# Kernel tuning notes

Measured on AMD Instinct MI355X. Metric: run time of the kernel, lower is better.

Reference implementation:

```python
import jax, jax.numpy as jnp
import numpy as np

B = 8
RESOLUTIONS = [65, 129, 257, 513, 1025]
NUM_POINTS = [0, 4096, 16384, 65536, 262144]
CLIP_MIN = -1e9
FINAL = 1025          # last resolution (both axes)
B_MIN, B_MAX = -1.0, 1.0
BALANCE = 0.5


def setup_inputs() -> dict:
    key = jax.random.key(0)
    k1, k2, k3, k4 = jax.random.split(key, 4)
    return {
        "w1": jax.random.normal(k1, (2, 256), jnp.float32),
        "b1": jax.random.normal(k2, (256,), jnp.float32),
        "w2": jax.random.normal(k3, (256, 1), jnp.float32),
        "b2": jax.random.normal(k4, (1,), jnp.float32),
    }


def _interp_bilinear_ac(x, H, W):
    """F.interpolate(..., mode='bilinear', align_corners=True). x: [B, C, h, w]."""
    b, c, h, w = x.shape
    ys = jnp.linspace(0.0, h - 1.0, H)
    xs = jnp.linspace(0.0, w - 1.0, W)
    y0 = jnp.floor(ys).astype(jnp.int32)
    y1 = jnp.minimum(y0 + 1, h - 1)
    wy = ys - y0
    x0 = jnp.floor(xs).astype(jnp.int32)
    x1 = jnp.minimum(x0 + 1, w - 1)
    wx = xs - x0
    # interpolate rows, then columns
    top = x[:, :, y0, :] * (1.0 - wy)[None, None, :, None] + x[:, :, y1, :] * wy[None, None, :, None]
    return top[:, :, :, x0] * (1.0 - wx) + top[:, :, :, x1] * wx


def _batch_eval(coords, w1, b1, w2, b2):
    """coords: [B, N, 2] in final-resolution pixel space (align_corners=False mapping).
    Returns occupancy [B, N] (C == 1)."""
    coords2d = coords / FINAL + 0.5 / FINAL                 # normalize to [0, 1]
    p = coords2d * (B_MAX - B_MIN) + B_MIN                  # [B, N, 2] in world coords
    h = jax.nn.relu(jnp.einsum('bnd,dh->bnh', p, w1) + b1)  # [B, N, 256]
    occ = jax.nn.sigmoid(jnp.einsum('bnh,ho->bno', h, w2) + b2)
    return occ[..., 0]


def reference(w1, b1, w2, b2):
    occ = None
    for i, res in enumerate(RESOLUTIONS):
        if i == 0:
            # init_coords: grid of res x res points spanning [0, FINAL-1]
            xs = jnp.linspace(0.0, FINAL - 1.0, res)
            gy, gx = jnp.meshgrid(xs, xs, indexing='ij')          # y rows, x cols
            coords = jnp.stack([gx.ravel(), gy.ravel()], axis=-1)  # [N, 2] (x, y)
            coords = jnp.broadcast_to(coords, (B, res * res, 2))
            o = _batch_eval(coords, w1, b1, w2, b2)               # [B, N]
            occ = o.reshape(B, 1, res, res)                       # [B, C, H, W]
        else:
            occ = _interp_bilinear_ac(occ, res, res)
            npt = NUM_POINTS[i]
            if npt <= 0:
                continue
            # uncertainty = -|occ - balance_value|
            unc = -jnp.abs(occ - BALANCE)                          # [B, 1, H, W]
            flat_unc = unc.reshape(B, res * res)
            scores, idx = jax.lax.top_k(flat_unc, npt)             # [B, npt]
            px = (idx % res).astype(jnp.float32)
            py = (idx // res).astype(jnp.float32)
            stride = (FINAL - 1.0) / (res - 1.0)
            coords = jnp.stack([px, py], axis=-1) * stride         # [B, npt, 2]
            new_vals = _batch_eval(coords, w1, b1, w2, b2)         # [B, npt]
            occ_flat = occ.reshape(B, res * res)
            old_vals = jnp.take_along_axis(occ_flat, idx, axis=1)
            vals = jnp.where(scores >= CLIP_MIN, new_vals, old_vals)
            occ_flat = jax.vmap(lambda o, i2, v: o.at[i2].set(v))(occ_flat, idx, vals)
            occ = occ_flat.reshape(B, 1, res, res)
    return occ
```

## Files before the change

### kernel.cpp

```cpp
#include <hip/hip_runtime.h>
#include <stdint.h>

#define HID 256
#define NMAXPIX (1025 * 1025)
#define NREP 8
#define NSEG 2048
#define SELMAX 2112

#define HISTA_OFF 0
#define HISTB_OFF 16384
#define HISTC_OFF 32768
#define SCAL_OFF  40960
#define TIC_OFF   41024
#define STAGE_U32 43072

__device__ __forceinline__ float mlp_eval4(float wx, float wy,
                                           const float4* __restrict__ w1x,
                                           const float4* __restrict__ w1y,
                                           const float4* __restrict__ vb1,
                                           const float4* __restrict__ vw2, float b2v) {
    const float C0 = (float)(0.5 / 1025.0);
    float px = (wx / 1025.0f + C0) * 2.0f - 1.0f;
    float py = (wy / 1025.0f + C0) * 2.0f - 1.0f;
    float a0 = 0.f, a1 = 0.f, a2 = 0.f, a3 = 0.f;
#pragma unroll 8
    for (int q = 0; q < HID / 4; ++q) {
        float4 a = w1x[q], b = w1y[q], c = vb1[q], d = vw2[q];
        float h0 = px * a.x + py * b.x + c.x;
        float h1 = px * a.y + py * b.y + c.y;
        float h2 = px * a.z + py * b.z + c.z;
        float h3 = px * a.w + py * b.w + c.w;
        h0 = h0 > 0.f ? h0 : 0.f;
        h1 = h1 > 0.f ? h1 : 0.f;
        h2 = h2 > 0.f ? h2 : 0.f;
        h3 = h3 > 0.f ? h3 : 0.f;
        a0 += h0 * d.x;
        a1 += h1 * d.y;
        a2 += h2 * d.z;
        a3 += h3 * d.w;
    }
    float x = ((a0 + a1) + (a2 + a3)) + b2v;
    float r;
    if (x >= 0.f) { r = 1.0f / (1.0f + expf(-x)); }
    else { float e = expf(x); r = e / (1.0f + e); }
    return r;
}

__device__ __forceinline__ uint32_t block_exscan_256(uint32_t v, volatile uint32_t* lds4) {
    int lane = threadIdx.x & 63, w = threadIdx.x >> 6;
    uint32_t inc = v;
#pragma unroll
    for (int d = 1; d < 64; d <<= 1) {
        uint32_t o = (uint32_t)__shfl_up((int)inc, d, 64);
        if (lane >= d) inc += o;
    }
    if (lane == 63) lds4[w] = inc;
    __syncthreads();
    uint32_t woff = 0;
    for (int i = 0; i < w; ++i) woff += lds4[i];
    return woff + inc - v;
}

__device__ void scan_dev(const uint32_t* __restrict__ hist, int NB,
                         uint32_t rem_in, uint32_t prefix_in, int shift,
                         uint32_t* outp, uint32_t* outr,
                         volatile uint32_t* lds4, volatile uint32_t* ldspair) {
    int tid = threadIdx.x;
    int C = NB >> 8;
    int b0 = NB - (tid + 1) * C;
    uint32_t cnts[8];
#pragma unroll
    for (int k = 0; k < 8; ++k) cnts[k] = 0;
    for (int rep = 0; rep < NREP; ++rep) {
        const uint4* p = (const uint4*)(hist + (size_t)rep * NB + b0);
#pragma unroll
        for (int g = 0; g < 2; ++g) {
            if (g * 4 < C) {
                uint4 v = p[g];
                cnts[g * 4 + 0] += v.x;
                cnts[g * 4 + 1] += v.y;
                cnts[g * 4 + 2] += v.z;
                cnts[g * 4 + 3] += v.w;
            }
        }
    }
    uint32_t ssum = 0;
    for (int k = 0; k < C; ++k) ssum += cnts[k];
    uint32_t excl = block_exscan_256(ssum, lds4);
    uint32_t run = excl;
    for (int k = 0; k < C; ++k) {
        uint32_t c = cnts[C - 1 - k];
        if (rem_in > run && rem_in <= run + c) {
            ldspair[0] = (prefix_in << shift) | (uint32_t)(b0 + C - 1 - k);
            ldspair[1] = rem_in - run;
        }
        run += c;
    }
    __syncthreads();
    *outp = ldspair[0];
    *outr = ldspair[1];
}

__global__ __launch_bounds__(256) void k_eval0z(const float* __restrict__ w1, const float* __restrict__ b1,
                                                const float* __restrict__ w2, const float* __restrict__ b2,
                                                float* __restrict__ occ, uint32_t* __restrict__ zbuf, int zcount) {
    __shared__ alignas(16) float sw1[2 * HID];
    __shared__ alignas(16) float sb1[HID];
    __shared__ alignas(16) float sw2[HID];
    int tid = threadIdx.x;
    for (int i = tid; i < 2 * HID; i += 256) sw1[i] = w1[i];
    sb1[tid] = b1[tid];
    sw2[tid] = w2[tid];
    __syncthreads();
    int gtid = blockIdx.x * 256 + tid;
    int nthreads = gridDim.x * 256;
    for (int i = gtid; i < zcount; i += nthreads) zbuf[i] = 0;
    for (int n = gtid; n < 65 * 65; n += nthreads) {
        int i = n / 65, j = n % 65;
        occ[n] = mlp_eval4(16.0f * (float)j, 16.0f * (float)i,
                           (const float4*)sw1, (const float4*)(sw1 + HID),
                           (const float4*)sb1, (const float4*)sw2, b2[0]);
    }
}

__global__ __launch_bounds__(256) void k_upkey(const float* __restrict__ in, int rp,
                                               float* __restrict__ outg, int r, int nb, int bstride,
                                               uint32_t* __restrict__ keys,
                                               uint32_t* __restrict__ histA) {
    __shared__ uint32_t hist[2048];
    int tid = threadIdx.x;
    for (int k = tid; k < 2048; k += 256) hist[k] = 0;
    __syncthreads();
    int N = r * r;
    int lane = tid & 63;
    int gstride = gridDim.x * 256;
    for (int n0 = blockIdx.x * 256; n0 < N; n0 += gstride) {
        int n = n0 + tid;
        bool act = n < N;
        uint32_t key = 0;
        if (act) {
            int i = n / r, j = n % r;
            int i2 = i >> 1, j2 = j >> 1;
            float v;
            if ((i & 1) == 0) {
                if ((j & 1) == 0) {
                    v = in[i2 * rp + j2];
                } else {
                    float a = in[i2 * rp + j2], b = in[i2 * rp + j2 + 1];
                    v = a * 0.5f + b * 0.5f;
                }
            } else {
                if ((j & 1) == 0) {
                    float a = in[i2 * rp + j2], b = in[(i2 + 1) * rp + j2];
                    v = a * 0.5f + b * 0.5f;
                } else {
                    float a = in[i2 * rp + j2],      c = in[i2 * rp + j2 + 1];
                    float b = in[(i2 + 1) * rp + j2], d = in[(i2 + 1) * rp + j2 + 1];
                    float t1 = a * 0.5f + b * 0.5f;
                    float t2 = c * 0.5f + d * 0.5f;
                    v = t1 * 0.5f + t2 * 0.5f;
                }
            }
            for (int k = 0; k < nb; ++k) outg[(size_t)k * bstride + n] = v;
            float unc = -fabsf(v - 0.5f);
            uint32_t u = __float_as_uint(unc);
            key = (u & 0x80000000u) ? ~u : (u | 0x80000000u);
            keys[n] = key;
        }
        uint32_t bin = key >> 21;
        unsigned long long m = __ballot(act);
        if (m) {
            int leader = __ffsll(m) - 1;
            uint32_t lbin = (uint32_t)__shfl((int)bin, leader, 64);
            unsigned long long smk = __ballot(act && bin == lbin);
            if (smk == m) {
                if (lane == leader) atomicAdd(&hist[lbin], (uint32_t)__popcll(m));
            } else if (act) {
                atomicAdd(&hist[bin], 1u);
            }
        }
    }
    __syncthreads();
    uint32_t* myrep = histA + (size_t)(blockIdx.x & (NREP - 1)) * 2048;
    for (int k = tid; k < 2048; k += 256) {
        uint32_t c = hist[k];
        if (c) atomicAdd(&myrep[k], c);
    }
}

__global__ __launch_bounds__(256) void k_histmid(const uint32_t* __restrict__ keys, int N,
                                                 const uint32_t* __restrict__ prevHist,
                                                 uint32_t* __restrict__ scal,
                                                 int useNpt, uint32_t npt, int scalInIdx, int shift,
                                                 int scalOutIdx,
                                                 int fshift, int bshift, uint32_t bmask,
                                                 uint32_t* __restrict__ outHist, int NBout) {
    __shared__ uint32_t lh[2048];
    __shared__ uint32_t lds4[4];
    __shared__ uint32_t ldspair[2];
    int tid = threadIdx.x, lane = tid & 63;
    uint32_t rem_in = useNpt ? npt : scal[scalInIdx + 1];
    uint32_t pfx_in = useNpt ? 0u  : scal[scalInIdx];
    uint32_t pfx, rem;
    scan_dev(prevHist, 2048, rem_in, pfx_in, shift, &pfx, &rem, lds4, ldspair);
    if (blockIdx.x == 0 && tid == 0) { scal[scalOutIdx] = pfx; scal[scalOutIdx + 1] = rem; }
    for (int k = tid; k < 2048; k += 256) lh[k] = 0;
    __syncthreads();
    int gstride = gridDim.x * 256;
    for (int base = blockIdx.x * 256; base < N; base += gstride) {
        int n = base + tid;
        bool inb = n < N;
        uint32_t key = inb ? keys[n] : 0u;
        bool flt = inb && ((key >> fshift) == pfx);
        uint32_t bin = (key >> bshift) & bmask;
        unsigned long long m = __ballot(flt);
        if (m) {
            int leader = __ffsll(m) - 1;
            uint32_t lbin = (uint32_t)__shfl((int)bin, leader, 64);
            unsigned long long smk = __ballot(flt && bin == lbin);
            if (smk == m) {
                if (lane == leader) atomicAdd(&lh[lbin], (uint32_t)__popcll(m));
            } else if (flt) {
                atomicAdd(&lh[bin], 1u);
            }
        }
    }
    __syncthreads();
    uint32_t* myrep = outHist + (size_t)(blockIdx.x & (NREP - 1)) * NBout;
    for (int k = tid; k < NBout; k += 256) {
        uint32_t c = lh[k];
        if (c) atomicAdd(&myrep[k], c);
    }
}

__global__ __launch_bounds__(256) void k_segcnt(const uint32_t* __restrict__ keys, int N, int seglen,
                                                const uint32_t* __restrict__ histC,
                                                uint32_t* __restrict__ scal,
                                                uint32_t* __restrict__ tic) {
    __shared__ uint32_t lds4[4];
    __shared__ uint32_t ldspair[2];
    int tid = threadIdx.x, lane = tid & 63;
    uint32_t rem2 = scal[3], pfx2 = scal[2];
    uint32_t K, t;
    scan_dev(histC, 1024, rem2, pfx2, 10, &K, &t, lds4, ldspair);
    if (blockIdx.x == 0 && tid == 0) { scal[4] = K; scal[5] = t; }
    int wv = blockIdx.x * 4 + (tid >> 6);
    int s0 = wv * seglen;
    int s1 = s0 + seglen; if (s1 > N) s1 = N;
    uint32_t tcnt = 0;
    for (int base = s0; base < s1; base += 64) {
        int n = base + lane;
        if (n < s1) tcnt += (keys[n] == K) ? 1u : 0u;
    }
#pragma unroll
    for (int d = 32; d; d >>= 1) tcnt += (uint32_t)__shfl_down((int)tcnt, d, 64);
    if (lane == 0) tic[wv] = tcnt;
}

__global__ __launch_bounds__(256) void k_seleval(const uint32_t* __restrict__ keys, int N, int seglen,
                                                 const uint32_t* __restrict__ scal,
                                                 const uint32_t* __restrict__ tic,
                                                 int r, float stride,
                                                 float* __restrict__ occ, int nb, int bstride,
                                                 const float* __restrict__ w1, const float* __restrict__ b1,
                                                 const float* __restrict__ w2, const float* __restrict__ b2) {
    __shared__ alignas(16) float sw1[2 * HID];
    __shared__ alignas(16) float sb1[HID];
    __shared__ alignas(16) float sw2[HID];
    __shared__ uint32_t selcnt;
    __shared__ uint32_t selidx[SELMAX];
    int tid = threadIdx.x, lane = tid & 63;
    for (int i = tid; i < 2 * HID; i += 256) sw1[i] = w1[i];
    sb1[tid] = b1[tid];
    sw2[tid] = w2[tid];
    if (tid == 0) selcnt = 0;
    __syncthreads();
    uint32_t K = scal[4], t = scal[5];

    int wv = blockIdx.x * 4 + (tid >> 6);
    uint32_t tp = 0;
    for (int i = lane; i < wv; i += 64) tp += tic[i];
#pragma unroll
    for (int d = 32; d; d >>= 1) tp += (uint32_t)__shfl_down((int)tp, d, 64);
    tp = (uint32_t)__shfl((int)tp, 0, 64);

    uint32_t tie_run = tp;
    int s0 = wv * seglen;
    int s1 = s0 + seglen; if (s1 > N) s1 = N;
    unsigned long long lowmask = (lane == 63) ? ~0ull >> 1 : ((1ull << lane) - 1ull);
    for (int base = s0; base < s1; base += 64) {
        int n = base + lane;
        bool inb = n < s1;
        uint32_t key = inb ? keys[n] : 0u;
        bool gt = inb && (key > K);
        bool tie = inb && (key == K);
        unsigned long long tm = __ballot(tie);
        uint32_t trank = tie_run + (uint32_t)__popcll(tm & lowmask);
        bool sel = gt || (tie && trank < t);
        unsigned long long smk = __ballot(sel);
        if (smk) {
            int leader = __ffsll(smk) - 1;
            uint32_t wbase = 0;
            if (lane == leader) wbase = atomicAdd(&selcnt, (uint32_t)__popcll(smk));
            wbase = (uint32_t)__shfl((int)wbase, leader, 64);
            if (sel) selidx[wbase + (uint32_t)__popcll(smk & lowmask)] = (uint32_t)n;
        }
        tie_run += (uint32_t)__popcll(tm);
    }
    __syncthreads();

    uint32_t cnt = selcnt;
    float vb2 = b2[0];
    const float4* w1x = (const float4*)sw1;
    const float4* w1y = (const float4*)(sw1 + HID);
    const float4* vb1 = (const float4*)sb1;
    const float4* vw2 = (const float4*)sw2;
    const float C0 = (float)(0.5 / 1025.0);
    for (uint32_t bb = 0; bb < cnt; bb += 512) {
        uint32_t i0 = bb + tid, i1 = bb + tid + 256;
        bool v0 = i0 < cnt, v1 = i1 < cnt;
        int nA = v0 ? (int)selidx[i0] : 0;
// ... 20 lines not shown
                A0.x += h0 * d.x; A0.y += h1 * d.y;
                A0.z += h2 * d.z; A0.w += h3 * d.w;
            }
            {
                float h0 = pxB * a.x + pyB * b.x + c.x;
                float h1 = pxB * a.y + pyB * b.y + c.y;
                float h2 = pxB * a.z + pyB * b.z + c.z;
                float h3 = pxB * a.w + pyB * b.w + c.w;
                h0 = h0 > 0.f ? h0 : 0.f;
                h1 = h1 > 0.f ? h1 : 0.f;
                h2 = h2 > 0.f ? h2 : 0.f;
                h3 = h3 > 0.f ? h3 : 0.f;
                A1.x += h0 * d.x; A1.y += h1 * d.y;
                A1.z += h2 * d.z; A1.w += h3 * d.w;
            }
        }
        if (v0) {
            float x = ((A0.x + A0.y) + (A0.z + A0.w)) + vb2;
            float rr;
            if (x >= 0.f) { rr = 1.0f / (1.0f + expf(-x)); }
            else { float e = expf(x); rr = e / (1.0f + e); }
            for (int k = 0; k < nb; ++k) occ[(size_t)k * bstride + nA] = rr;
        }
        if (v1) {
            float x = ((A1.x + A1.y) + (A1.z + A1.w)) + vb2;
            float rr;
            if (x >= 0.f) { rr = 1.0f / (1.0f + expf(-x)); }
            else { float e = expf(x); rr = e / (1.0f + e); }
            for (int k = 0; k < nb; ++k) occ[(size_t)k * bstride + nB] = rr;
        }
    }
}

__global__ __launch_bounds__(256) void k_bcast(const float* __restrict__ src, float* __restrict__ dst, int N) {
    int q = blockIdx.x * 256 + threadIdx.x;
    int n = q * 4;
    if (n + 3 < N) {
        float4 v = *(const float4*)(src + n);
#pragma unroll
        for (int k = 0; k < 8; ++k) *(float4*)(dst + (size_t)k * N + n) = v;
    } else if (n < N) {
        for (int m = n; m < N; ++m) {
            float v = src[m];
#pragma unroll
            for (int k = 0; k < 8; ++k) dst[(size_t)k * N + m] = v;
        }
    }
}

extern "C" void kernel_launch(void* const* d_in, const int* in_sizes, int n_in,
                              void* d_out, int out_size, void* d_ws, size_t ws_size,
                              hipStream_t stream) {
    const float* w1 = (const float*)d_in[0];
    const float* b1 = (const float*)d_in[1];
    const float* w2 = (const float*)d_in[2];
    const float* b2 = (const float*)d_in[3];
    float* out = (float*)d_out;

    const size_t A = (((size_t)NMAXPIX * 4) + 255) & ~(size_t)255;
    const size_t SMALL_BYTES = (size_t)4 * STAGE_U32 * 4;
    const size_t need = 3 * A + SMALL_BYTES;

    int fused8 = (ws_size >= need);
    char* base = fused8 ? (char*)d_ws : (char*)d_out;
    float* buf0 = (float*)(base);
    float* buf1 = (float*)(base + A);
    uint32_t* keys = (uint32_t*)(base + 2 * A);
    uint32_t* smallb = (uint32_t*)(base + 3 * A);

    k_eval0z<<<dim3(512), dim3(256), 0, stream>>>(w1, b1, w2, b2, buf0, smallb, 4 * STAGE_U32);

    const int resA[5] = {65, 129, 257, 513, 1025};
    const int nptA[5] = {0, 4096, 16384, 65536, 262144};
    float* cur = buf0;
    float* nxt = buf1;
    for (int s = 1; s < 5; ++s) {
        int rp = resA[s - 1], r = resA[s];
        int N = r * r;
        uint32_t npt = (uint32_t)nptA[s];
        uint32_t* sm    = smallb + (size_t)(s - 1) * STAGE_U32;
        uint32_t* histA = sm + HISTA_OFF;
        uint32_t* histB = sm + HISTB_OFF;
        uint32_t* histC = sm + HISTC_OFF;
        uint32_t* scal  = sm + SCAL_OFF;
        uint32_t* tic   = sm + TIC_OFF;
        int nb1 = (N + 255) / 256;
        int nbu = nb1 < 1024 ? nb1 : 1024;
        int seglen = (N + NSEG - 1) / NSEG;
        float stride = 1024.0f / (float)(r - 1);

        int last = (s == 4);
        float* stage_out = (last && fused8) ? out : nxt;
        int nb = (last && fused8) ? 8 : 1;
        int bstride = (last && fused8) ? NMAXPIX : 0;

        k_upkey<<<dim3(nbu), dim3(256), 0, stream>>>(cur, rp, stage_out, r, nb, bstride, keys, histA);
        k_histmid<<<dim3(512), dim3(256), 0, stream>>>(keys, N, histA, scal, 1, npt, 0, 0,
                                                       0, 21, 10, 0x7FFu, histB, 2048);
        k_histmid<<<dim3(512), dim3(256), 0, stream>>>(keys, N, histB, scal, 0, 0u, 0, 11,
                                                       2, 10, 0, 0x3FFu, histC, 1024);
        k_segcnt<<<dim3(NSEG / 4), dim3(256), 0, stream>>>(keys, N, seglen, histC, scal, tic);
        k_seleval<<<dim3(NSEG / 4), dim3(256), 0, stream>>>(keys, N, seglen, scal, tic, r, stride,
                                                            stage_out, nb, bstride, w1, b1, w2, b2);
        if (!(last && fused8)) { float* tmp = cur; cur = nxt; nxt = tmp; }
    }
    if (!fused8) {
        k_bcast<<<dim3(((NMAXPIX + 3) / 4 + 255) / 256), dim3(256), 0, stream>>>(cur, out, NMAXPIX);
    }
}
```

Baseline: 244.6 us.

## Fuse stage-1 selection into one block and merge segcnt with seleval via decoupled lookback

Stage 1 (129x129) now runs its upsample, three-pass radix select and tie counting in a single-block kernel, replacing four grid-wide launches with one. For the later stages, the segment-count and select-eval kernels are merged into one kernel. That kernel computes its tie prefix with a decoupled-lookback scan over per-block flags, and falls back to recounting a segment if a predecessor has not published within a spin limit. The aim is to cut kernel launches and inter-kernel gaps. In exchange it relies on inter-block spin-waiting and a recount fallback, which add complexity and can cost time when predecessor blocks are slow to publish.

```diff
diff --git a/kernel.cpp b/kernel.cpp
--- a/kernel.cpp
+++ b/kernel.cpp
@@ -61,17 +61,17 @@
     return woff + inc - v;
 }
 
-__device__ void scan_dev(const uint32_t* __restrict__ hist, int NB,
-                         uint32_t rem_in, uint32_t prefix_in, int shift,
-                         uint32_t* outp, uint32_t* outr,
-                         volatile uint32_t* lds4, volatile uint32_t* ldspair) {
+__device__ void scan_generic(const uint32_t* __restrict__ hist, int NB, int nrep,
+                             uint32_t rem_in, uint32_t prefix_in, int shift,
+                             uint32_t* outp, uint32_t* outr,
+                             volatile uint32_t* lds4, volatile uint32_t* ldspair) {
     int tid = threadIdx.x;
     int C = NB >> 8;
     int b0 = NB - (tid + 1) * C;
     uint32_t cnts[8];
 #pragma unroll
     for (int k = 0; k < 8; ++k) cnts[k] = 0;
-    for (int rep = 0; rep < NREP; ++rep) {
+    for (int rep = 0; rep < nrep; ++rep) {
         const uint4* p = (const uint4*)(hist + (size_t)rep * NB + b0);
 #pragma unroll
         for (int g = 0; g < 2; ++g) {
@@ -99,6 +99,46 @@
     __syncthreads();
     *outp = ldspair[0];
     *outr = ldspair[1];
+}
+
+__device__ __forceinline__ void hist_add(uint32_t* lh, uint32_t bin, bool act, int lane) {
+    unsigned long long m = __ballot(act);
+    if (m) {
+        int leader = __ffsll(m) - 1;
+        uint32_t lbin = (uint32_t)__shfl((int)bin, leader, 64);
+        unsigned long long smk = __ballot(act && bin == lbin);
+        if (smk == m) {
+            if (lane == leader) atomicAdd(&lh[lbin], (uint32_t)__popcll(m));
+        } else if (act) {
+            atomicAdd(&lh[bin], 1u);
+        }
+    }
+}
+
+__device__ __forceinline__ float up2x(const float* __restrict__ in, int rp, int r, int n) {
+    int i = n / r, j = n % r;
+    int i2 = i >> 1, j2 = j >> 1;
+    float v;
+    if ((i & 1) == 0) {
+        if ((j & 1) == 0) {
+            v = in[i2 * rp + j2];
+        } else {
+            float a = in[i2 * rp + j2], b = in[i2 * rp + j2 + 1];
+            v = a * 0.5f + b * 0.5f;
+        }
+    } else {
+        if ((j & 1) == 0) {
+            float a = in[i2 * rp + j2], b = in[(i2 + 1) * rp + j2];
+            v = a * 0.5f + b * 0.5f;
+        } else {
+            float a = in[i2 * rp + j2],      c = in[i2 * rp + j2 + 1];
+            float b = in[(i2 + 1) * rp + j2], d = in[(i2 + 1) * rp + j2 + 1];
+            float t1 = a * 0.5f + b * 0.5f;
+            float t2 = c * 0.5f + d * 0.5f;
+            v = t1 * 0.5f + t2 * 0.5f;
+        }
+    }
+    return v;
 }
 
 __global__ __launch_bounds__(256) void k_eval0z(const float* __restrict__ w1, const float* __restrict__ b1,
@@ -123,6 +163,60 @@
     }
 }
 
+__global__ __launch_bounds__(256) void k_sel1(const float* __restrict__ in,
+                                              float* __restrict__ outg,
+                                              uint32_t* __restrict__ keys,
+                                              uint32_t* __restrict__ scal,
+                                              uint32_t* __restrict__ tic) {
+    __shared__ alignas(16) uint32_t lh[2048];
+    __shared__ uint32_t lds4[4];
+    __shared__ uint32_t ldspair[2];
+    const int rp = 65, r = 129, N = 129 * 129;
+    const uint32_t npt = 4096;
+    const int seglen = 9;
+    int tid = threadIdx.x;
+    for (int k = tid; k < 2048; k += 256) lh[k] = 0;
+    __syncthreads();
+    for (int n = tid; n < N; n += 256) {
+        float v = up2x(in, rp, r, n);
+        outg[n] = v;
+        float unc = -fabsf(v - 0.5f);
+        uint32_t u = __float_as_uint(unc);
+        uint32_t key = (u & 0x80000000u) ? ~u : (u | 0x80000000u);
+        keys[n] = key;
+        atomicAdd(&lh[key >> 21], 1u);
+    }
+    __syncthreads();
+    uint32_t pfx1, rem1;
+    scan_generic(lh, 2048, 1, npt, 0u, 0, &pfx1, &rem1, lds4, ldspair);
+    for (int k = tid; k < 2048; k += 256) lh[k] = 0;
+    __syncthreads();
+    for (int n = tid; n < N; n += 256) {
+        uint32_t key = keys[n];
+        if ((key >> 21) == pfx1) atomicAdd(&lh[(key >> 10) & 0x7FFu], 1u);
+    }
+    __syncthreads();
+    uint32_t pfx2, rem2;
+    scan_generic(lh, 2048, 1, rem1, pfx1, 11, &pfx2, &rem2, lds4, ldspair);
+    for (int k = tid; k < 2048; k += 256) lh[k] = 0;
+    __syncthreads();
+    for (int n = tid; n < N; n += 256) {
+        uint32_t key = keys[n];
+        if ((key >> 10) == pfx2) atomicAdd(&lh[key & 0x3FFu], 1u);
+    }
+    __syncthreads();
+    uint32_t K, t;
+    scan_generic(lh, 1024, 1, rem2, pfx2, 10, &K, &t, lds4, ldspair);
+    if (tid == 0) { scal[4] = K; scal[5] = t; }
+    for (int k = tid; k < 2048; k += 256) lh[k] = 0;
+    __syncthreads();
+    for (int n = tid; n < N; n += 256) {
+        if (keys[n] == K) atomicAdd(&lh[(uint32_t)n / (uint32_t)seglen], 1u);
+    }
+    __syncthreads();
+    for (int k = tid; k < 2048; k += 256) tic[k] = lh[k];
+}
+
 __global__ __launch_bounds__(256) void k_upkey(const float* __restrict__ in, int rp,
                                                float* __restrict__ outg, int r, int nb, int bstride,
                                                uint32_t* __restrict__ keys,
@@ -139,46 +233,14 @@
         bool act = n < N;
         uint32_t key = 0;
         if (act) {
-            int i = n / r, j = n % r;
-            int i2 = i >> 1, j2 = j >> 1;
-            float v;
-            if ((i & 1) == 0) {
-                if ((j & 1) == 0) {
-                    v = in[i2 * rp + j2];
-                } else {
-                    float a = in[i2 * rp + j2], b = in[i2 * rp + j2 + 1];
-                    v = a * 0.5f + b * 0.5f;
-                }
-            } else {
-                if ((j & 1) == 0) {
-                    float a = in[i2 * rp + j2], b = in[(i2 + 1) * rp + j2];
-                    v = a * 0.5f + b * 0.5f;
-                } else {
-                    float a = in[i2 * rp + j2],      c = in[i2 * rp + j2 + 1];
-                    float b = in[(i2 + 1) * rp + j2], d = in[(i2 + 1) * rp + j2 + 1];
-                    float t1 = a * 0.5f + b * 0.5f;
-                    float t2 = c * 0.5f + d * 0.5f;
-                    v = t1 * 0.5f + t2 * 0.5f;
-                }
-            }
+            float v = up2x(in, rp, r, n);
             for (int k = 0; k < nb; ++k) outg[(size_t)k * bstride + n] = v;
             float unc = -fabsf(v - 0.5f);
             uint32_t u = __float_as_uint(unc);
             key = (u & 0x80000000u) ? ~u : (u | 0x80000000u);
             keys[n] = key;
         }
-        uint32_t bin = key >> 21;
-        unsigned long long m = __ballot(act);
-        if (m) {
-            int leader = __ffsll(m) - 1;
-            uint32_t lbin = (uint32_t)__shfl((int)bin, leader, 64);
-            unsigned long long smk = __ballot(act && bin == lbin);
-            if (smk == m) {
-                if (lane == leader) atomicAdd(&hist[lbin], (uint32_t)__popcll(m));
-            } else if (act) {
-                atomicAdd(&hist[bin], 1u);
-            }
-        }
+        hist_add(hist, key >> 21, act, lane);
     }
     __syncthreads();
     uint32_t* myrep = histA + (size_t)(blockIdx.x & (NREP - 1)) * 2048;
@@ -202,7 +264,7 @@
     uint32_t rem_in = useNpt ? npt : scal[scalInIdx + 1];
     uint32_t pfx_in = useNpt ? 0u  : scal[scalInIdx];
     uint32_t pfx, rem;
-    scan_dev(prevHist, 2048, rem_in, pfx_in, shift, &pfx, &rem, lds4, ldspair);
+    scan_generic(prevHist, 2048, NREP, rem_in, pfx_in, shift, &pfx, &rem, lds4, ldspair);
     if (blockIdx.x == 0 && tid == 0) { scal[scalOutIdx] = pfx; scal[scalOutIdx + 1] = rem; }
     for (int k = tid; k < 2048; k += 256) lh[k] = 0;
     __syncthreads();
@@ -213,17 +275,7 @@
         uint32_t key = inb ? keys[n] : 0u;
         bool flt = inb && ((key >> fshift) == pfx);
         uint32_t bin = (key >> bshift) & bmask;
-        unsigned long long m = __ballot(flt);
-        if (m) {
-            int leader = __ffsll(m) - 1;
-            uint32_t lbin = (uint32_t)__shfl((int)bin, leader, 64);
-            unsigned long long smk = __ballot(flt && bin == lbin);
-            if (smk == m) {
-                if (lane == leader) atomicAdd(&lh[lbin], (uint32_t)__popcll(m));
-            } else if (flt) {
-                atomicAdd(&lh[bin], 1u);
-            }
-        }
+        hist_add(lh, bin, flt, lane);
     }
     __syncthreads();
     uint32_t* myrep = outHist + (size_t)(blockIdx.x & (NREP - 1)) * NBout;
@@ -233,18 +285,35 @@
     }
 }
 
-__global__ __launch_bounds__(256) void k_segcnt(const uint32_t* __restrict__ keys, int N, int seglen,
-                                                const uint32_t* __restrict__ histC,
-                                                uint32_t* __restrict__ scal,
-                                                uint32_t* __restrict__ tic) {
+__global__ __launch_bounds__(256, 2) void k_segsel(
+        const uint32_t* __restrict__ keys, int N, int seglen,
+        const uint32_t* __restrict__ histC,
+        const uint32_t* __restrict__ scal,
+        uint32_t* __restrict__ tic,
+        int r, float stride,
+        float* __restrict__ occ, int nb, int bstride,
+        const float* __restrict__ w1, const float* __restrict__ b1,
+        const float* __restrict__ w2, const float* __restrict__ b2) {
+    __shared__ alignas(16) float sw1[2 * HID];
+    __shared__ alignas(16) float sb1[HID];
+    __shared__ alignas(16) float sw2[HID];
+    __shared__ uint32_t selcnt;
+    __shared__ uint32_t selidx[SELMAX];
     __shared__ uint32_t lds4[4];
     __shared__ uint32_t ldspair[2];
-    int tid = threadIdx.x, lane = tid & 63;
+    __shared__ uint32_t wtc[4];
+    __shared__ uint32_t s_excl;
+    int tid = threadIdx.x, lane = tid & 63, w = tid >> 6;
+    for (int i = tid; i < 2 * HID; i += 256) sw1[i] = w1[i];
+    sb1[tid] = b1[tid];
+    sw2[tid] = w2[tid];
+    if (tid == 0) selcnt = 0;
+
     uint32_t rem2 = scal[3], pfx2 = scal[2];
     uint32_t K, t;
-    scan_dev(histC, 1024, rem2, pfx2, 10, &K, &t, lds4, ldspair);
-    if (blockIdx.x == 0 && tid == 0) { scal[4] = K; scal[5] = t; }
-    int wv = blockIdx.x * 4 + (tid >> 6);
+    scan_generic(histC, 1024, NREP, rem2, pfx2, 10, &K, &t, lds4, ldspair);
+
+    int wv = blockIdx.x * 4 + w;
     int s0 = wv * seglen;
     int s1 = s0 + seglen; if (s1 > N) s1 = N;
     uint32_t tcnt = 0;
@@ -254,39 +323,68 @@
     }
 #pragma unroll
     for (int d = 32; d; d >>= 1) tcnt += (uint32_t)__shfl_down((int)tcnt, d, 64);
-    if (lane == 0) tic[wv] = tcnt;
-}
-
-__global__ __launch_bounds__(256) void k_seleval(const uint32_t* __restrict__ keys, int N, int seglen,
-                                                 const uint32_t* __restrict__ scal,
-                                                 const uint32_t* __restrict__ tic,
-                                                 int r, float stride,
-                                                 float* __restrict__ occ, int nb, int bstride,
-                                                 const float* __restrict__ w1, const float* __restrict__ b1,
-                                                 const float* __restrict__ w2, const float* __restrict__ b2) {
-    __shared__ alignas(16) float sw1[2 * HID];
-    __shared__ alignas(16) float sb1[HID];
-    __shared__ alignas(16) float sw2[HID];
-    __shared__ uint32_t selcnt;
-    __shared__ uint32_t selidx[SELMAX];
-    int tid = threadIdx.x, lane = tid & 63;
-    for (int i = tid; i < 2 * HID; i += 256) sw1[i] = w1[i];
-    sb1[tid] = b1[tid];
-    sw2[tid] = w2[tid];
-    if (tid == 0) selcnt = 0;
-    __syncthreads();
-    uint32_t K = scal[4], t = scal[5];
-
-    int wv = blockIdx.x * 4 + (tid >> 6);
-    uint32_t tp = 0;
-    for (int i = lane; i < wv; i += 64) tp += tic[i];
-#pragma unroll
-    for (int d = 32; d; d >>= 1) tp += (uint32_t)__shfl_down((int)tp, d, 64);
-    tp = (uint32_t)__shfl((int)tp, 0, 64);
-
-    uint32_t tie_run = tp;
-    int s0 = wv * seglen;
-    int s1 = s0 + seglen; if (s1 > N) s1 = N;
+    if (lane == 0) wtc[w] = tcnt;
+    __syncthreads();
+    uint32_t agg = wtc[0] + wtc[1] + wtc[2] + wtc[3];
+    uint32_t intra = 0;
+    for (int i = 0; i < w; ++i) intra += wtc[i];
+
+    if (tid == 0) {
+        uint32_t st = (blockIdx.x == 0) ? ((2u << 30) | agg) : ((1u << 30) | agg);
+        __hip_atomic_store(&tic[blockIdx.x], st, __ATOMIC_RELAXED, __HIP_MEMORY_SCOPE_AGENT);
+        if (blockIdx.x == 0) s_excl = 0;
+    }
+    if (blockIdx.x > 0 && w == 0) {
+        uint32_t excl = 0;
+        int b = (int)blockIdx.x - 1;
+        for (;;) {
+            int mine = b - lane;
+            bool active = (mine >= 0);
+            uint32_t f = 0;
+            if (active) {
+                f = __hip_atomic_load(&tic[mine], __ATOMIC_RELAXED, __HIP_MEMORY_SCOPE_AGENT);
+                int spins = 0;
+                while ((f >> 30) == 0u && spins < 200) {
+                    __builtin_amdgcn_s_sleep(2);
+                    f = __hip_atomic_load(&tic[mine], __ATOMIC_RELAXED, __HIP_MEMORY_SCOPE_AGENT);
+                    ++spins;
+                }
+                if ((f >> 30) == 0u) {
+                    int ms0 = mine * seglen;
+                    int ms1 = ms0 + seglen; if (ms1 > N) ms1 = N;
+                    uint32_t c = 0;
+                    for (int n2 = ms0; n2 < ms1; ++n2) c += (keys[n2] == K) ? 1u : 0u;
+                    f = (1u << 30) | c;
+                }
+            }
+            unsigned long long incm = __ballot(active && (f >> 30) == 2u);
+            uint32_t val;
+            bool done = (incm != 0ull);
+            if (done) {
+                int l2 = __ffsll(incm) - 1;
+                val = (lane <= l2) ? (f & 0x3FFFFFFFu) : 0u;
+            } else {
+                val = active ? (f & 0x3FFFFFFFu) : 0u;
+            }
+#pragma unroll
+            for (int d = 32; d; d >>= 1) val += (uint32_t)__shfl_down((int)val, d, 64);
+            val = (uint32_t)__shfl((int)val, 0, 64);
+            excl += val;
+            if (done || b < 64) {
+                if (!done) break;
+                break;
+            }
+            b -= 64;
+        }
+        if (lane == 0) {
+            __hip_atomic_store(&tic[blockIdx.x], (2u << 30) | (excl + agg),
+                               __ATOMIC_RELAXED, __HIP_MEMORY_SCOPE_AGENT);
+            s_excl = excl;
+        }
+    }
+    __syncthreads();
+    uint32_t tie_run = s_excl + intra;
+
     unsigned long long lowmask = (lane == 63) ? ~0ull >> 1 : ((1ull << lane) - 1ull);
     for (int base = s0; base < s1; base += 64) {
         int n = base + lane;
@@ -373,6 +471,122 @@
     }
 }
 
+__global__ __launch_bounds__(256) void k_seleval(const uint32_t* __restrict__ keys, int N, int seglen,
+                                                 const uint32_t* __restrict__ scal,
+                                                 const uint32_t* __restrict__ tic,
+                                                 int r, float stride,
+                                                 float* __restrict__ occ, int nb, int bstride,
+                                                 const float* __restrict__ w1, const float* __restrict__ b1,
+                                                 const float* __restrict__ w2, const float* __restrict__ b2) {
+    __shared__ alignas(16) float sw1[2 * HID];
+    __shared__ alignas(16) float sb1[HID];
+    __shared__ alignas(16) float sw2[HID];
+    __shared__ uint32_t selcnt;
+    __shared__ uint32_t selidx[SELMAX];
+    int tid = threadIdx.x, lane = tid & 63;
+    for (int i = tid; i < 2 * HID; i += 256) sw1[i] = w1[i];
+    sb1[tid] = b1[tid];
+    sw2[tid] = w2[tid];
+    if (tid == 0) selcnt = 0;
+    __syncthreads();
+    uint32_t K = scal[4], t = scal[5];
+
+    int wv = blockIdx.x * 4 + (tid >> 6);
+    uint32_t tp = 0;
+    for (int i = lane; i < wv; i += 64) tp += tic[i];
+#pragma unroll
+    for (int d = 32; d; d >>= 1) tp += (uint32_t)__shfl_down((int)tp, d, 64);
+    tp = (uint32_t)__shfl((int)tp, 0, 64);
+
+    uint32_t tie_run = tp;
+    int s0 = wv * seglen;
+    int s1 = s0 + seglen; if (s1 > N) s1 = N;
+    unsigned long long lowmask = (lane == 63) ? ~0ull >> 1 : ((1ull << lane) - 1ull);
+    for (int base = s0; base < s1; base += 64) {
+        int n = base + lane;
+        bool inb = n < s1;
+        uint32_t key = inb ? keys[n] : 0u;
+        bool gt = inb && (key > K);
+        bool tie = inb && (key == K);
+        unsigned long long tm = __ballot(tie);
+        uint32_t trank = tie_run + (uint32_t)__popcll(tm & lowmask);
+        bool sel = gt || (tie && trank < t);
+        unsigned long long smk = __ballot(sel);
+        if (smk) {
+            int leader = __ffsll(smk) - 1;
+            uint32_t wbase = 0;
+            if (lane == leader) wbase = atomicAdd(&selcnt, (uint32_t)__popcll(smk));
+            wbase = (uint32_t)__shfl((int)wbase, leader, 64);
+            if (sel) selidx[wbase + (uint32_t)__popcll(smk & lowmask)] = (uint32_t)n;
+        }
+        tie_run += (uint32_t)__popcll(tm);
+    }
+    __syncthreads();
+
+    uint32_t cnt = selcnt;
+    float vb2 = b2[0];
+    const float4* w1x = (const float4*)sw1;
+    const float4* w1y = (const float4*)(sw1 + HID);
+    const float4* vb1 = (const float4*)sb1;
+    const float4* vw2 = (const float4*)sw2;
+    const float C0 = (float)(0.5 / 1025.0);
+    for (uint32_t bb = 0; bb < cnt; bb += 512) {
+        uint32_t i0 = bb + tid, i1 = bb + tid + 256;
+        bool v0 = i0 < cnt, v1 = i1 < cnt;
+        int nA = v0 ? (int)selidx[i0] : 0;
+        int nB = v1 ? (int)selidx[i1] : 0;
+        int iA = nA / r, jA = nA % r;
+        int iB = nB / r, jB = nB % r;
+        float pxA = ((stride * (float)jA) / 1025.0f + C0) * 2.0f - 1.0f;
+        float pyA = ((stride * (float)iA) / 1025.0f + C0) * 2.0f - 1.0f;
+        float pxB = ((stride * (float)jB) / 1025.0f + C0) * 2.0f - 1.0f;
+        float pyB = ((stride * (float)iB) / 1025.0f + C0) * 2.0f - 1.0f;
+        float4 A0 = {0, 0, 0, 0}, A1 = {0, 0, 0, 0};
+#pragma unroll 4
+        for (int q = 0; q < HID / 4; ++q) {
+            float4 a = w1x[q], b = w1y[q], c = vb1[q], d = vw2[q];
+            {
+                float h0 = pxA * a.x + pyA * b.x + c.x;
+                float h1 = pxA * a.y + pyA * b.y + c.y;
+                float h2 = pxA * a.z + pyA * b.z + c.z;
+                float h3 = pxA * a.w + pyA * b.w + c.w;
+                h0 = h0 > 0.f ? h0 : 0.f;
+                h1 = h1 > 0.f ? h1 : 0.f;
+                h2 = h2 > 0.f ? h2 : 0.f;
+                h3 = h3 > 0.f ? h3 : 0.f;
+                A0.x += h0 * d.x; A0.y += h1 * d.y;
+                A0.z += h2 * d.z; A0.w += h3 * d.w;
+            }
+            {
+                float h0 = pxB * a.x + pyB * b.x + c.x;
+                float h1 = pxB * a.y + pyB * b.y + c.y;
+                float h2 = pxB * a.z + pyB * b.z + c.z;
+                float h3 = pxB * a.w + pyB * b.w + c.w;
+                h0 = h0 > 0.f ? h0 : 0.f;
+                h1 = h1 > 0.f ? h1 : 0.f;
+                h2 = h2 > 0.f ? h2 : 0.f;
+                h3 = h3 > 0.f ? h3 : 0.f;
+                A1.x += h0 * d.x; A1.y += h1 * d.y;
+                A1.z += h2 * d.z; A1.w += h3 * d.w;
+            }
+        }
+        if (v0) {
+            float x = ((A0.x + A0.y) + (A0.z + A0.w)) + vb2;
+            float rr;
+            if (x >= 0.f) { rr = 1.0f / (1.0f + expf(-x)); }
+            else { float e = expf(x); rr = e / (1.0f + e); }
+            for (int k = 0; k < nb; ++k) occ[(size_t)k * bstride + nA] = rr;
+        }
+        if (v1) {
+            float x = ((A1.x + A1.y) + (A1.z + A1.w)) + vb2;
+            float rr;
+            if (x >= 0.f) { rr = 1.0f / (1.0f + expf(-x)); }
+            else { float e = expf(x); rr = e / (1.0f + e); }
+            for (int k = 0; k < nb; ++k) occ[(size_t)k * bstride + nB] = rr;
+        }
+    }
+}
+
 __global__ __launch_bounds__(256) void k_bcast(const float* __restrict__ src, float* __restrict__ dst, int N) {
     int q = blockIdx.x * 256 + threadIdx.x;
     int n = q * 4;
@@ -411,11 +625,21 @@
 
     k_eval0z<<<dim3(512), dim3(256), 0, stream>>>(w1, b1, w2, b2, buf0, smallb, 4 * STAGE_U32);
 
+    {
+        uint32_t* sm = smallb;
+        uint32_t* scal = sm + SCAL_OFF;
+        uint32_t* tic  = sm + TIC_OFF;
+        const int N1 = 129 * 129;
+        k_sel1<<<dim3(1), dim3(256), 0, stream>>>(buf0, buf1, keys, scal, tic);
+        k_seleval<<<dim3(NSEG / 4), dim3(256), 0, stream>>>(keys, N1, 9, scal, tic, 129, 8.0f,
+                                                            buf1, 1, 0, w1, b1, w2, b2);
+    }
+
     const int resA[5] = {65, 129, 257, 513, 1025};
     const int nptA[5] = {0, 4096, 16384, 65536, 262144};
-    float* cur = buf0;
-    float* nxt = buf1;
-    for (int s = 1; s < 5; ++s) {
+    float* cur = buf1;
+    float* nxt = buf0;
+    for (int s = 2; s < 5; ++s) {
         int rp = resA[s - 1], r = resA[s];
         int N = r * r;
         uint32_t npt = (uint32_t)nptA[s];
@@ -440,9 +664,9 @@
                                                        0, 21, 10, 0x7FFu, histB, 2048);
         k_histmid<<<dim3(512), dim3(256), 0, stream>>>(keys, N, histB, scal, 0, 0u, 0, 11,
                                                        2, 10, 0, 0x3FFu, histC, 1024);
-        k_segcnt<<<dim3(NSEG / 4), dim3(256), 0, stream>>>(keys, N, seglen, histC, scal, tic);
-        k_seleval<<<dim3(NSEG / 4), dim3(256), 0, stream>>>(keys, N, seglen, scal, tic, r, stride,
-                                                            stage_out, nb, bstride, w1, b1, w2, b2);
+        k_segsel<<<dim3(NSEG / 4), dim3(256), 0, stream>>>(keys, N, seglen, histC, scal, tic,
+                                                           r, stride, stage_out, nb, bstride,
+                                                           w1, b1, w2, b2);
         if (!(last && fused8)) { float* tmp = cur; cur = nxt; nxt = tmp; }
     }
     if (!fused8) {
```

New measurement: 296.2 us. 21.1% more time.

## Fuse per-stage radix-select kernels into one persistent kernel with grid barriers

Applied to the files above, without the earlier changes.

Merges the five per-stage kernels (upsample+key histogram, two mid histogram passes, segment tie count, select+eval) into a single 512-block kernel. Stages synchronise through global atomic counters with spin-wait barriers, and the tie prefix uses a decoupled look-back across blocks. This removes about four launches per stage and keeps each block's key chunk hot in cache. In exchange it depends on all 512 blocks being co-resident, and it has slow redundant fallback paths for when a spin times out.

```diff
diff --git a/kernel.cpp b/kernel.cpp
--- a/kernel.cpp
+++ b/kernel.cpp
@@ -6,6 +6,7 @@
 #define NREP 8
 #define NSEG 2048
 #define SELMAX 2112
+#define NBLK 512
 
 #define HISTA_OFF 0
 #define HISTB_OFF 16384
@@ -61,17 +62,17 @@
     return woff + inc - v;
 }
 
-__device__ void scan_dev(const uint32_t* __restrict__ hist, int NB,
-                         uint32_t rem_in, uint32_t prefix_in, int shift,
-                         uint32_t* outp, uint32_t* outr,
-                         volatile uint32_t* lds4, volatile uint32_t* ldspair) {
+__device__ void scan_generic(const uint32_t* __restrict__ hist, int NB, int nrep,
+                             uint32_t rem_in, uint32_t prefix_in, int shift,
+                             uint32_t* outp, uint32_t* outr,
+                             volatile uint32_t* lds4, volatile uint32_t* ldspair) {
     int tid = threadIdx.x;
     int C = NB >> 8;
     int b0 = NB - (tid + 1) * C;
     uint32_t cnts[8];
 #pragma unroll
     for (int k = 0; k < 8; ++k) cnts[k] = 0;
-    for (int rep = 0; rep < NREP; ++rep) {
+    for (int rep = 0; rep < nrep; ++rep) {
         const uint4* p = (const uint4*)(hist + (size_t)rep * NB + b0);
 #pragma unroll
         for (int g = 0; g < 2; ++g) {
@@ -99,6 +100,73 @@
     __syncthreads();
     *outp = ldspair[0];
     *outr = ldspair[1];
+}
+
+__device__ __forceinline__ void hist_add(uint32_t* lh, uint32_t bin, bool act, int lane) {
+    unsigned long long m = __ballot(act);
+    if (m) {
+        int leader = __ffsll(m) - 1;
+        uint32_t lbin = (uint32_t)__shfl((int)bin, leader, 64);
+        unsigned long long smk = __ballot(act && bin == lbin);
+        if (smk == m) {
+            if (lane == leader) atomicAdd(&lh[lbin], (uint32_t)__popcll(m));
+        } else if (act) {
+            atomicAdd(&lh[bin], 1u);
+        }
+    }
+}
+
+__device__ __forceinline__ float up2x(const float* __restrict__ in, int rp, int r, int n) {
+    int i = n / r, j = n % r;
+    int i2 = i >> 1, j2 = j >> 1;
+    float v;
+    if ((i & 1) == 0) {
+        if ((j & 1) == 0) {
+            v = in[i2 * rp + j2];
+        } else {
+            float a = in[i2 * rp + j2], b = in[i2 * rp + j2 + 1];
+            v = a * 0.5f + b * 0.5f;
+        }
+    } else {
+        if ((j & 1) == 0) {
+            float a = in[i2 * rp + j2], b = in[(i2 + 1) * rp + j2];
+            v = a * 0.5f + b * 0.5f;
+        } else {
+            float a = in[i2 * rp + j2],      c = in[i2 * rp + j2 + 1];
+            float b = in[(i2 + 1) * rp + j2], d = in[(i2 + 1) * rp + j2 + 1];
+            float t1 = a * 0.5f + b * 0.5f;
+            float t2 = c * 0.5f + d * 0.5f;
+            v = t1 * 0.5f + t2 * 0.5f;
+        }
+    }
+    return v;
+}
+
+__device__ __forceinline__ uint32_t key_of(const float* __restrict__ in, int rp, int r, int n) {
+    float v = up2x(in, rp, r, n);
+    float unc = -fabsf(v - 0.5f);
+    uint32_t u = __float_as_uint(unc);
+    return (u & 0x80000000u) ? ~u : (u | 0x80000000u);
+}
+
+__device__ bool wait_all(uint32_t* ctr, uint32_t target, volatile uint32_t* sflag) {
+    if (threadIdx.x == 0) {
+        uint32_t d = __hip_atomic_load(ctr, __ATOMIC_RELAXED, __HIP_MEMORY_SCOPE_AGENT);
+        int spins = 0;
+        while (d < target && spins < 30000) {
+            __builtin_amdgcn_s_sleep(8);
+            d = __hip_atomic_load(ctr, __ATOMIC_RELAXED, __HIP_MEMORY_SCOPE_AGENT);
+            ++spins;
+        }
+        if (d >= target) {
+            (void)__hip_atomic_load(ctr, __ATOMIC_ACQUIRE, __HIP_MEMORY_SCOPE_AGENT);
+            *sflag = 1;
+        } else {
+            *sflag = 0;
+        }
+    }
+    __syncthreads();
+    return *sflag != 0;
 }
 
 __global__ __launch_bounds__(256) void k_eval0z(const float* __restrict__ w1, const float* __restrict__ b1,
@@ -123,128 +191,146 @@
     }
 }
 
-__global__ __launch_bounds__(256) void k_upkey(const float* __restrict__ in, int rp,
-                                               float* __restrict__ outg, int r, int nb, int bstride,
-                                               uint32_t* __restrict__ keys,
-                                               uint32_t* __restrict__ histA) {
-    __shared__ uint32_t hist[2048];
-    int tid = threadIdx.x;
-    for (int k = tid; k < 2048; k += 256) hist[k] = 0;
-    __syncthreads();
-    int N = r * r;
-    int lane = tid & 63;
-    int gstride = gridDim.x * 256;
-    for (int n0 = blockIdx.x * 256; n0 < N; n0 += gstride) {
+__global__ __launch_bounds__(256, 2) void k_stage(
+        const float* __restrict__ in, int rp, int r, int N, uint32_t npt,
+        float* __restrict__ occ, int nb, int bstride, float stride,
+        uint32_t* __restrict__ keys, uint32_t* __restrict__ sm,
+        const float* __restrict__ w1, const float* __restrict__ b1,
+        const float* __restrict__ w2, const float* __restrict__ b2) {
+    __shared__ alignas(16) float sw1[2 * HID];
+    __shared__ alignas(16) float sb1[HID];
+    __shared__ alignas(16) float sw2[HID];
+    __shared__ alignas(16) uint32_t lh[2048];
+    __shared__ uint32_t selidx[SELMAX];
+    __shared__ uint32_t selcnt;
+    __shared__ uint32_t lds4[4];
+    __shared__ uint32_t ldspair[2];
+    __shared__ uint32_t wtc[4];
+    __shared__ uint32_t s_excl;
+    __shared__ uint32_t sflag;
+
+    uint32_t* histA = sm + HISTA_OFF;
+    uint32_t* histB = sm + HISTB_OFF;
+    uint32_t* histC = sm + HISTC_OFF;
+    uint32_t* scal  = sm + SCAL_OFF;
+    uint32_t* tic   = sm + TIC_OFF;
+
+    const int tid = threadIdx.x, lane = tid & 63, w = tid >> 6;
+    const int seglen = (N + NSEG - 1) / NSEG;
+    const int c0 = blockIdx.x * 4 * seglen;
+    int c1 = c0 + 4 * seglen; if (c1 > N) c1 = N;
+
+    for (int i = tid; i < 2 * HID; i += 256) sw1[i] = w1[i];
+    sb1[tid] = b1[tid];
+    sw2[tid] = w2[tid];
+    if (tid == 0) { selcnt = 0; s_excl = 0; }
+    for (int k = tid; k < 2048; k += 256) lh[k] = 0;
+    __syncthreads();
+
+    for (int n0 = c0; n0 < c1; n0 += 256) {
         int n = n0 + tid;
-        bool act = n < N;
+        bool act = n < c1;
         uint32_t key = 0;
         if (act) {
-            int i = n / r, j = n % r;
-            int i2 = i >> 1, j2 = j >> 1;
-            float v;
-            if ((i & 1) == 0) {
-                if ((j & 1) == 0) {
-                    v = in[i2 * rp + j2];
-                } else {
-                    float a = in[i2 * rp + j2], b = in[i2 * rp + j2 + 1];
-                    v = a * 0.5f + b * 0.5f;
-                }
-            } else {
-                if ((j & 1) == 0) {
-                    float a = in[i2 * rp + j2], b = in[(i2 + 1) * rp + j2];
-                    v = a * 0.5f + b * 0.5f;
-                } else {
-                    float a = in[i2 * rp + j2],      c = in[i2 * rp + j2 + 1];
-                    float b = in[(i2 + 1) * rp + j2], d = in[(i2 + 1) * rp + j2 + 1];
-                    float t1 = a * 0.5f + b * 0.5f;
-                    float t2 = c * 0.5f + d * 0.5f;
-                    v = t1 * 0.5f + t2 * 0.5f;
-                }
-            }
-            for (int k = 0; k < nb; ++k) outg[(size_t)k * bstride + n] = v;
+            float v = up2x(in, rp, r, n);
+            for (int k = 0; k < nb; ++k) occ[(size_t)k * bstride + n] = v;
             float unc = -fabsf(v - 0.5f);
             uint32_t u = __float_as_uint(unc);
             key = (u & 0x80000000u) ? ~u : (u | 0x80000000u);
             keys[n] = key;
         }
-        uint32_t bin = key >> 21;
-        unsigned long long m = __ballot(act);
-        if (m) {
-            int leader = __ffsll(m) - 1;
-            uint32_t lbin = (uint32_t)__shfl((int)bin, leader, 64);
-            unsigned long long smk = __ballot(act && bin == lbin);
-            if (smk == m) {
-                if (lane == leader) atomicAdd(&hist[lbin], (uint32_t)__popcll(m));
-            } else if (act) {
-                atomicAdd(&hist[bin], 1u);
-            }
-        }
-    }
-    __syncthreads();
-    uint32_t* myrep = histA + (size_t)(blockIdx.x & (NREP - 1)) * 2048;
-    for (int k = tid; k < 2048; k += 256) {
-        uint32_t c = hist[k];
-        if (c) atomicAdd(&myrep[k], c);
-    }
-}
-
-__global__ __launch_bounds__(256) void k_histmid(const uint32_t* __restrict__ keys, int N,
-                                                 const uint32_t* __restrict__ prevHist,
-                                                 uint32_t* __restrict__ scal,
-                                                 int useNpt, uint32_t npt, int scalInIdx, int shift,
-                                                 int scalOutIdx,
-                                                 int fshift, int bshift, uint32_t bmask,
-                                                 uint32_t* __restrict__ outHist, int NBout) {
-    __shared__ uint32_t lh[2048];
-    __shared__ uint32_t lds4[4];
-    __shared__ uint32_t ldspair[2];
-    int tid = threadIdx.x, lane = tid & 63;
-    uint32_t rem_in = useNpt ? npt : scal[scalInIdx + 1];
-    uint32_t pfx_in = useNpt ? 0u  : scal[scalInIdx];
-    uint32_t pfx, rem;
-    scan_dev(prevHist, 2048, rem_in, pfx_in, shift, &pfx, &rem, lds4, ldspair);
-    if (blockIdx.x == 0 && tid == 0) { scal[scalOutIdx] = pfx; scal[scalOutIdx + 1] = rem; }
+        hist_add(lh, key >> 21, act, lane);
+    }
+    __syncthreads();
+    {
+        uint32_t* rep = histA + (size_t)(blockIdx.x & (NREP - 1)) * 2048;
+        for (int k = tid; k < 2048; k += 256) { uint32_t c = lh[k]; if (c) atomicAdd(&rep[k], c); }
+    }
+    __syncthreads();
+    if (tid == 0) __hip_atomic_fetch_add(&scal[8], 1u, __ATOMIC_RELEASE, __HIP_MEMORY_SCOPE_AGENT);
+
+    uint32_t pfx1, rem1;
+    if (wait_all(&scal[8], NBLK, &sflag)) {
+        scan_generic(histA, 2048, NREP, npt, 0u, 0, &pfx1, &rem1, lds4, ldspair);
+    } else {
+        for (int k = tid; k < 2048; k += 256) lh[k] = 0;
+        __syncthreads();
+        for (int n0 = 0; n0 < N; n0 += 256) {
+            int n = n0 + tid; bool act = n < N;
+            uint32_t key = act ? key_of(in, rp, r, n) : 0u;
+            hist_add(lh, key >> 21, act, lane);
+        }
+        __syncthreads();
+        scan_generic(lh, 2048, 1, npt, 0u, 0, &pfx1, &rem1, lds4, ldspair);
+    }
+
     for (int k = tid; k < 2048; k += 256) lh[k] = 0;
     __syncthreads();
-    int gstride = gridDim.x * 256;
-    for (int base = blockIdx.x * 256; base < N; base += gstride) {
-        int n = base + tid;
-        bool inb = n < N;
-        uint32_t key = inb ? keys[n] : 0u;
-        bool flt = inb && ((key >> fshift) == pfx);
-        uint32_t bin = (key >> bshift) & bmask;
-        unsigned long long m = __ballot(flt);
-        if (m) {
-            int leader = __ffsll(m) - 1;
-            uint32_t lbin = (uint32_t)__shfl((int)bin, leader, 64);
-            unsigned long long smk = __ballot(flt && bin == lbin);
-            if (smk == m) {
-                if (lane == leader) atomicAdd(&lh[lbin], (uint32_t)__popcll(m));
-            } else if (flt) {
-                atomicAdd(&lh[bin], 1u);
-            }
-        }
-    }
-    __syncthreads();
-    uint32_t* myrep = outHist + (size_t)(blockIdx.x & (NREP - 1)) * NBout;
-    for (int k = tid; k < NBout; k += 256) {
-        uint32_t c = lh[k];
-        if (c) atomicAdd(&myrep[k], c);
-    }
-}
-
-__global__ __launch_bounds__(256) void k_segcnt(const uint32_t* __restrict__ keys, int N, int seglen,
-                                                const uint32_t* __restrict__ histC,
-                                                uint32_t* __restrict__ scal,
-                                                uint32_t* __restrict__ tic) {
-    __shared__ uint32_t lds4[4];
-    __shared__ uint32_t ldspair[2];
-    int tid = threadIdx.x, lane = tid & 63;
-    uint32_t rem2 = scal[3], pfx2 = scal[2];
+    for (int n0 = c0; n0 < c1; n0 += 256) {
+        int n = n0 + tid;
+        bool act = n < c1;
+        uint32_t key = act ? keys[n] : 0u;
+        bool flt = act && ((key >> 21) == pfx1);
+        hist_add(lh, (key >> 10) & 0x7FFu, flt, lane);
+    }
+    __syncthreads();
+    {
+        uint32_t* rep = histB + (size_t)(blockIdx.x & (NREP - 1)) * 2048;
+        for (int k = tid; k < 2048; k += 256) { uint32_t c = lh[k]; if (c) atomicAdd(&rep[k], c); }
+    }
+    __syncthreads();
+    if (tid == 0) __hip_atomic_fetch_add(&scal[9], 1u, __ATOMIC_RELEASE, __HIP_MEMORY_SCOPE_AGENT);
+
+    uint32_t pfx2, rem2;
+    if (wait_all(&scal[9], NBLK, &sflag)) {
+        scan_generic(histB, 2048, NREP, rem1, pfx1, 11, &pfx2, &rem2, lds4, ldspair);
+    } else {
+        for (int k = tid; k < 2048; k += 256) lh[k] = 0;
+        __syncthreads();
+        for (int n0 = 0; n0 < N; n0 += 256) {
+            int n = n0 + tid; bool act = n < N;
+            uint32_t key = act ? key_of(in, rp, r, n) : 0u;
+            bool flt = act && ((key >> 21) == pfx1);
+            hist_add(lh, (key >> 10) & 0x7FFu, flt, lane);
+        }
+        __syncthreads();
+        scan_generic(lh, 2048, 1, rem1, pfx1, 11, &pfx2, &rem2, lds4, ldspair);
+    }
+
+    for (int k = tid; k < 2048; k += 256) lh[k] = 0;
+    __syncthreads();
+    for (int n0 = c0; n0 < c1; n0 += 256) {
+        int n = n0 + tid;
+        bool act = n < c1;
+        uint32_t key = act ? keys[n] : 0u;
+        bool flt = act && ((key >> 10) == pfx2);
+        hist_add(lh, key & 0x3FFu, flt, lane);
+    }
+    __syncthreads();
+    {
+        uint32_t* rep = histC + (size_t)(blockIdx.x & (NREP - 1)) * 1024;
+        for (int k = tid; k < 1024; k += 256) { uint32_t c = lh[k]; if (c) atomicAdd(&rep[k], c); }
+    }
+    __syncthreads();
+    if (tid == 0) __hip_atomic_fetch_add(&scal[10], 1u, __ATOMIC_RELEASE, __HIP_MEMORY_SCOPE_AGENT);
+
     uint32_t K, t;
-    scan_dev(histC, 1024, rem2, pfx2, 10, &K, &t, lds4, ldspair);
-    if (blockIdx.x == 0 && tid == 0) { scal[4] = K; scal[5] = t; }
-    int wv = blockIdx.x * 4 + (tid >> 6);
+    if (wait_all(&scal[10], NBLK, &sflag)) {
+        scan_generic(histC, 1024, NREP, rem2, pfx2, 10, &K, &t, lds4, ldspair);
+    } else {
+        for (int k = tid; k < 2048; k += 256) lh[k] = 0;
+        __syncthreads();
+        for (int n0 = 0; n0 < N; n0 += 256) {
+            int n = n0 + tid; bool act = n < N;
+            uint32_t key = act ? key_of(in, rp, r, n) : 0u;
+            bool flt = act && ((key >> 10) == pfx2);
+            hist_add(lh, key & 0x3FFu, flt, lane);
+        }
+        __syncthreads();
+        scan_generic(lh, 1024, 1, rem2, pfx2, 10, &K, &t, lds4, ldspair);
+    }
+
+    int wv = blockIdx.x * 4 + w;
     int s0 = wv * seglen;
     int s1 = s0 + seglen; if (s1 > N) s1 = N;
     uint32_t tcnt = 0;
@@ -254,39 +340,65 @@
     }
 #pragma unroll
     for (int d = 32; d; d >>= 1) tcnt += (uint32_t)__shfl_down((int)tcnt, d, 64);
-    if (lane == 0) tic[wv] = tcnt;
-}
-
-__global__ __launch_bounds__(256) void k_seleval(const uint32_t* __restrict__ keys, int N, int seglen,
-                                                 const uint32_t* __restrict__ scal,
-                                                 const uint32_t* __restrict__ tic,
-                                                 int r, float stride,
-                                                 float* __restrict__ occ, int nb, int bstride,
-                                                 const float* __restrict__ w1, const float* __restrict__ b1,
-                                                 const float* __restrict__ w2, const float* __restrict__ b2) {
-    __shared__ alignas(16) float sw1[2 * HID];
-    __shared__ alignas(16) float sb1[HID];
-    __shared__ alignas(16) float sw2[HID];
-    __shared__ uint32_t selcnt;
-    __shared__ uint32_t selidx[SELMAX];
-    int tid = threadIdx.x, lane = tid & 63;
-    for (int i = tid; i < 2 * HID; i += 256) sw1[i] = w1[i];
-    sb1[tid] = b1[tid];
-    sw2[tid] = w2[tid];
-    if (tid == 0) selcnt = 0;
-    __syncthreads();
-    uint32_t K = scal[4], t = scal[5];
-
-    int wv = blockIdx.x * 4 + (tid >> 6);
-    uint32_t tp = 0;
-    for (int i = lane; i < wv; i += 64) tp += tic[i];
-#pragma unroll
-    for (int d = 32; d; d >>= 1) tp += (uint32_t)__shfl_down((int)tp, d, 64);
-    tp = (uint32_t)__shfl((int)tp, 0, 64);
-
-    uint32_t tie_run = tp;
-    int s0 = wv * seglen;
-    int s1 = s0 + seglen; if (s1 > N) s1 = N;
+    if (lane == 0) wtc[w] = tcnt;
+    __syncthreads();
+    uint32_t agg = wtc[0] + wtc[1] + wtc[2] + wtc[3];
+    uint32_t intra = 0;
+    for (int i = 0; i < w; ++i) intra += wtc[i];
+
+    if (tid == 0) {
+        uint32_t st = (blockIdx.x == 0) ? ((2u << 30) | agg) : ((1u << 30) | agg);
+        __hip_atomic_store(&tic[blockIdx.x], st, __ATOMIC_RELAXED, __HIP_MEMORY_SCOPE_AGENT);
+    }
+    if (blockIdx.x > 0 && w == 0) {
+        uint32_t excl = 0;
+        int b = (int)blockIdx.x - 1;
+        for (;;) {
+            int mine = b - lane;
+            bool active = (mine >= 0);
+            uint32_t f = 0;
+            if (active) {
+                f = __hip_atomic_load(&tic[mine], __ATOMIC_RELAXED, __HIP_MEMORY_SCOPE_AGENT);
+                int spins = 0;
+                while ((f >> 30) == 0u && spins < 1000) {
+                    __builtin_amdgcn_s_sleep(2);
+                    f = __hip_atomic_load(&tic[mine], __ATOMIC_RELAXED, __HIP_MEMORY_SCOPE_AGENT);
+                    ++spins;
+                }
+                if ((f >> 30) == 0u) {
+                    int ms0 = mine * seglen;
+                    int ms1 = ms0 + seglen; if (ms1 > N) ms1 = N;
+                    uint32_t c = 0;
+                    for (int n2 = ms0; n2 < ms1; ++n2) c += (key_of(in, rp, r, n2) == K) ? 1u : 0u;
+                    f = (1u << 30) | c;
+                }
+            }
+            unsigned long long incm = __ballot(active && (f >> 30) == 2u);
+            uint32_t val;
+            bool done = (incm != 0ull);
+            if (done) {
+                int l2 = __ffsll(incm) - 1;
+                val = (lane <= l2) ? (f & 0x3FFFFFFFu) : 0u;
+            } else {
+                val = active ? (f & 0x3FFFFFFFu) : 0u;
+            }
+#pragma unroll
+            for (int d = 32; d; d >>= 1) val += (uint32_t)__shfl_down((int)val, d, 64);
+            val = (uint32_t)__shfl((int)val, 0, 64);
+            excl += val;
+            if (done) break;
+            if (b < 64) break;
+            b -= 64;
+        }
+        if (lane == 0) {
+            __hip_atomic_store(&tic[blockIdx.x], (2u << 30) | (excl + agg),
+                               __ATOMIC_RELAXED, __HIP_MEMORY_SCOPE_AGENT);
+            s_excl = excl;
+        }
+    }
+    __syncthreads();
+    uint32_t tie_run = s_excl + intra;
+
     unsigned long long lowmask = (lane == 63) ? ~0ull >> 1 : ((1ull << lane) - 1ull);
     for (int base = s0; base < s1; base += 64) {
         int n = base + lane;
@@ -419,15 +531,7 @@
         int rp = resA[s - 1], r = resA[s];
         int N = r * r;
         uint32_t npt = (uint32_t)nptA[s];
-        uint32_t* sm    = smallb + (size_t)(s - 1) * STAGE_U32;
-        uint32_t* histA = sm + HISTA_OFF;
-        uint32_t* histB = sm + HISTB_OFF;
-        uint32_t* histC = sm + HISTC_OFF;
-        uint32_t* scal  = sm + SCAL_OFF;
-        uint32_t* tic   = sm + TIC_OFF;
-        int nb1 = (N + 255) / 256;
-        int nbu = nb1 < 1024 ? nb1 : 1024;
-        int seglen = (N + NSEG - 1) / NSEG;
+        uint32_t* sm = smallb + (size_t)(s - 1) * STAGE_U32;
         float stride = 1024.0f / (float)(r - 1);
 
         int last = (s == 4);
@@ -435,14 +539,9 @@
         int nb = (last && fused8) ? 8 : 1;
         int bstride = (last && fused8) ? NMAXPIX : 0;
 
-        k_upkey<<<dim3(nbu), dim3(256), 0, stream>>>(cur, rp, stage_out, r, nb, bstride, keys, histA);
-        k_histmid<<<dim3(512), dim3(256), 0, stream>>>(keys, N, histA, scal, 1, npt, 0, 0,
-                                                       0, 21, 10, 0x7FFu, histB, 2048);
-        k_histmid<<<dim3(512), dim3(256), 0, stream>>>(keys, N, histB, scal, 0, 0u, 0, 11,
-                                                       2, 10, 0, 0x3FFu, histC, 1024);
-        k_segcnt<<<dim3(NSEG / 4), dim3(256), 0, stream>>>(keys, N, seglen, histC, scal, tic);
-        k_seleval<<<dim3(NSEG / 4), dim3(256), 0, stream>>>(keys, N, seglen, scal, tic, r, stride,
-                                                            stage_out, nb, bstride, w1, b1, w2, b2);
+        k_stage<<<dim3(NBLK), dim3(256), 0, stream>>>(cur, rp, r, N, npt,
+                                                      stage_out, nb, bstride, stride,
+                                                      keys, sm, w1, b1, w2, b2);
         if (!(last && fused8)) { float* tmp = cur; cur = nxt; nxt = tmp; }
     }
     if (!fused8) {
```

After: 582.9 us. 138% more time.
